# Kernel optimization log

Hardware: AMD Instinct MI355X
Metric: run time of the kernel (lower is better)

## Reference

```python
import jax, jax.numpy as jnp
import numpy as np

N, E, D, H = 50000, 800000, 128, 8
C = D // H  # per-head out_channels = 16
NEG_SLOPE = 0.2
EPS = 1e-5


def _layer_norm(x, w):
    mu = x.mean(-1, keepdims=True)
    var = ((x - mu) ** 2).mean(-1, keepdims=True)
    return (x - mu) / jnp.sqrt(var + EPS) * w


def setup_inputs() -> dict:
    key = jax.random.key(0)
    ks = jax.random.split(key, 9)
    s = 0.05  # weight init scale
    return {
        "x": jax.random.normal(ks[0], (N, D), dtype=jnp.float32),
        "edge_index": jax.random.randint(ks[1], (2, E), 0, N, dtype=jnp.int32),
        "edge_attr": jax.random.normal(ks[2], (E, D), dtype=jnp.float32),
        "ln1_w": jnp.ones((D,), jnp.float32),
        "lin_l_w": jax.random.normal(ks[3], (D, D), dtype=jnp.float32) * s,
        "lin_l_b": jnp.zeros((D,), jnp.float32),
        "lin_r_w": jax.random.normal(ks[4], (D, D), dtype=jnp.float32) * s,
        "lin_r_b": jnp.zeros((D,), jnp.float32),
        "lin_edge_w": jax.random.normal(ks[5], (D, D), dtype=jnp.float32) * s,
        "att": jax.random.normal(ks[6], (H, C), dtype=jnp.float32) * s,
        "attn_bias": jnp.zeros((D,), jnp.float32),
        "ln2_w": jnp.ones((D,), jnp.float32),
        "fc_w": jax.random.normal(ks[7], (4 * D, D), dtype=jnp.float32) * s,
        "proj_w": jax.random.normal(ks[8], (D, 4 * D), dtype=jnp.float32) * s,
    }


def reference(x, edge_index, edge_attr, ln1_w, lin_l_w, lin_l_b, lin_r_w,
              lin_r_b, lin_edge_w, att, attn_bias, ln2_w, fc_w, proj_w):
    n, d = x.shape
    h_heads, c = att.shape
    # --- GATv2Conv on ln_1(x) ---
    h = _layer_norm(x, ln1_w)
    xl = (h @ lin_l_w.T + lin_l_b).reshape(n, h_heads, c)  # source transform
    xr = (h @ lin_r_w.T + lin_r_b).reshape(n, h_heads, c)  # target transform
    e = (edge_attr @ lin_edge_w.T).reshape(-1, h_heads, c)  # [E,H,C]
    src, dst = edge_index[0], edge_index[1]
    z = jax.nn.leaky_relu(xl[src] + xr[dst] + e, NEG_SLOPE)  # [E,H,C]
    logits = jnp.einsum('ehc,hc->eh', z, att)  # [E,H]
    # segment softmax over destination nodes
    m = jax.lax.stop_gradient(jax.ops.segment_max(logits, dst, num_segments=n))
    num = jnp.exp(logits - m[dst])
    den = jax.ops.segment_sum(num, dst, num_segments=n)
    alpha = num / den[dst]  # [E,H]
    msg = xl[src] * alpha[..., None]  # [E,H,C]
    attn_out = jax.ops.segment_sum(msg, dst, num_segments=n).reshape(n, d) + attn_bias
    x = x + attn_out
    # --- MLP on ln_2(x) ---
    h2 = _layer_norm(x, ln2_w)
    x = x + jax.nn.relu(h2 @ fc_w.T) @ proj_w.T
    return x
```

## Files before the change

### kernel.cpp

```cpp
#include <hip/hip_runtime.h>

#define D 128
#define HEADS 8
#define CH 16
#define NEG 0.2f
#define LNEPS 1e-5f

typedef __attribute__((ext_vector_type(8))) short bf16x8;
typedef __attribute__((ext_vector_type(4))) float f32x4;

#define MFMA(a, b, c) __builtin_amdgcn_mfma_f32_16x16x32_bf16(a, b, c, 0, 0, 0)

__device__ __forceinline__ short f2bf(float f) {
    unsigned u = __builtin_bit_cast(unsigned, f);
    unsigned r = (u + 0x7fffu + ((u >> 16) & 1u)) >> 16;
    return (short)r;
}
__device__ __forceinline__ float bflo(unsigned u) {
    return __builtin_bit_cast(float, u << 16);
}
__device__ __forceinline__ float bfhi(unsigned u) {
    return __builtin_bit_cast(float, u & 0xffff0000u);
}
__device__ __forceinline__ bf16x8 pack8(f32x4 lo, f32x4 hi) {
    bf16x8 r;
    r[0] = f2bf(lo[0]); r[1] = f2bf(lo[1]); r[2] = f2bf(lo[2]); r[3] = f2bf(lo[3]);
    r[4] = f2bf(hi[0]); r[5] = f2bf(hi[1]); r[6] = f2bf(hi[2]); r[7] = f2bf(hi[3]);
    return r;
}

__global__ void convert_weights(const float* __restrict__ wl, const float* __restrict__ wr,
                                const float* __restrict__ we, const float* __restrict__ fc,
                                const float* __restrict__ pj, short* __restrict__ out) {
    int idx = blockIdx.x * 256 + threadIdx.x;
    float v;
    if (idx < 16384) v = wl[idx];
    else if (idx < 32768) v = wr[idx - 16384];
    else if (idx < 49152) v = we[idx - 32768];
    else if (idx < 114688) v = fc[idx - 49152];
    else if (idx < 180224) v = pj[idx - 114688];
    else return;
    out[idx] = f2bf(v);
}

__global__ void ln_kernel(const float* __restrict__ x, const float* __restrict__ w,
                          short* __restrict__ h, int n) {
    int row = blockIdx.x * 4 + (threadIdx.x >> 6);
    if (row >= n) return;
    int l = threadIdx.x & 63;
    long base = (long)row * D;
    float a = x[base + l], b = x[base + l + 64];
    float s = a + b, ss = a * a + b * b;
    #pragma unroll
    for (int m = 1; m < 64; m <<= 1) { s += __shfl_xor(s, m); ss += __shfl_xor(ss, m); }
    float mu = s * (1.0f / 128.0f);
    float var = ss * (1.0f / 128.0f) - mu * mu;
    float rstd = rsqrtf(var + LNEPS);
    h[base + l]      = f2bf((a - mu) * rstd * w[l]);
    h[base + l + 64] = f2bf((b - mu) * rstd * w[l + 64]);
}

__global__ __launch_bounds__(256) void node_lin_kernel(
        const short* __restrict__ h, const short* __restrict__ wl, const short* __restrict__ wr,
        const float* __restrict__ bl, const float* __restrict__ br,
        short* __restrict__ xl, short* __restrict__ xr, int n) {
    int wave = threadIdx.x >> 6, l = threadIdx.x & 63;
    int rbase = blockIdx.x * 64 + wave * 16;
    int g = l >> 4, c = l & 15;
    f32x4 acc[16];
    #pragma unroll
    for (int t = 0; t < 16; t++) acc[t] = (f32x4){0.f, 0.f, 0.f, 0.f};
    int arow = rbase + c;
    #pragma unroll
    for (int kk = 0; kk < 4; kk++) {
        int k0 = kk * 32 + g * 8;
        bf16x8 af = {};
        if (arow < n) af = *(const bf16x8*)(h + (long)arow * D + k0);
        #pragma unroll
        for (int t = 0; t < 16; t++) {
            const short* w = (t < 8) ? wl : wr;
            int col = (t & 7) * 16 + c;
            bf16x8 bf = *(const bf16x8*)(w + col * D + k0);
            acc[t] = MFMA(af, bf, acc[t]);
        }
    }
    #pragma unroll
    for (int t = 0; t < 16; t++) {
        int col = (t & 7) * 16 + c;
        short* out = (t < 8) ? xl : xr;
        float bias = (t < 8) ? bl[col] : br[col];
        #pragma unroll
        for (int r = 0; r < 4; r++) {
            int row = rbase + g * 4 + r;
            if (row < n) out[(long)row * D + col] = f2bf(acc[t][r] + bias);
        }
    }
}

__global__ void hist_kernel(const int* __restrict__ dst, int* __restrict__ counts, int nE) {
    int e = blockIdx.x * 256 + threadIdx.x;
    if (e < nE) atomicAdd(&counts[dst[e]], 1);
}

__global__ void scan1_kernel(const int* __restrict__ counts, int* __restrict__ offsets,
                             int* __restrict__ blocksum, int n) {
    __shared__ int sd[1024];
    int tid = threadIdx.x;
    int gid = blockIdx.x * 1024 + tid;
    int v = (gid < n) ? counts[gid] : 0;
    sd[tid] = v;
    __syncthreads();
    int acc = v;
    #pragma unroll
    for (int off = 1; off < 1024; off <<= 1) {
        int t = (tid >= off) ? sd[tid - off] : 0;
        __syncthreads();
        acc += t;
        sd[tid] = acc;
        __syncthreads();
    }
    if (gid < n) offsets[gid] = acc - v;
    if (tid == 1023) blocksum[blockIdx.x] = acc;
}

__global__ void scan2_kernel(int* __restrict__ blocksum, int nb) {
    __shared__ int sd[256];
    int tid = threadIdx.x;
    int v = (tid < nb) ? blocksum[tid] : 0;
    sd[tid] = v;
    __syncthreads();
    int acc = v;
    #pragma unroll
    for (int off = 1; off < 256; off <<= 1) {
        int t = (tid >= off) ? sd[tid - off] : 0;
        __syncthreads();
        acc += t;
        sd[tid] = acc;
        __syncthreads();
    }
    if (tid < nb) blocksum[tid] = acc - v;
}

__global__ void scan3_kernel(int* __restrict__ offsets, const int* __restrict__ blocksum,
                             int* __restrict__ cursor, int n) {
    int gid = blockIdx.x * 256 + threadIdx.x;
    if (gid < n) {
        int o = offsets[gid] + blocksum[gid >> 10];
        offsets[gid] = o;
        cursor[gid] = o;
    }
}

__global__ void place_kernel(const int* __restrict__ src, const int* __restrict__ dst,
                             int* __restrict__ cursor, int* __restrict__ src_perm,
                             int* __restrict__ dst_perm, int* __restrict__ eid_perm,
                             int nE) {
    int e = blockIdx.x * 256 + threadIdx.x;
    if (e < nE) {
        int d = dst[e];
        int pos = atomicAdd(&cursor[d], 1);
        src_perm[pos] = src[e];
        dst_perm[pos] = d;
        eid_perm[pos] = e;
    }
}

__global__ __launch_bounds__(256) void edge_kernel(
        const float* __restrict__ ea, const short* __restrict__ we,
        const int* __restrict__ src_perm, const int* __restrict__ dst_perm,
        const int* __restrict__ eid_perm,
        const short* __restrict__ xl, const short* __restrict__ xr,
        const float* __restrict__ att, float* __restrict__ num_perm,
        int nE, int ntiles, int nwaves) {
    __shared__ short wlds[16384];
    int tid = threadIdx.x;

    {
        int row = tid >> 1, half = tid & 1;
        const short* srow = we + row * D + half * 64;
        #pragma unroll
        for (int j = 0; j < 8; j++) {
            bf16x8 v = *(const bf16x8*)(srow + j * 8);
            int off = (half * 128 + j * 16) ^ ((row & 15) << 4);
            *(bf16x8*)((char*)wlds + row * 256 + off) = v;
        }
    }
    __syncthreads();

    int wave = tid >> 6, l = tid & 63;
    int el = l & 15, g = l >> 4;
    long ti = (long)blockIdx.x * 4 + wave;
    if (ti >= ntiles) return;

    int sp, dp;
    f32x4 ear[8];
    {
        long p0 = ti * 16 + el;
        long pc = (p0 < nE) ? p0 : (nE - 1);
        sp = src_perm[pc]; dp = dst_perm[pc];
        long ep = eid_perm[pc];
        const float* p = ea + ep * D + g * 8;
        ear[0] = *(const f32x4*)(p);       ear[1] = *(const f32x4*)(p + 4);
        ear[2] = *(const f32x4*)(p + 32);  ear[3] = *(const f32x4*)(p + 36);
        ear[4] = *(const f32x4*)(p + 64);  ear[5] = *(const f32x4*)(p + 68);
        ear[6] = *(const f32x4*)(p + 96);  ear[7] = *(const f32x4*)(p + 100);
    }

    for (; ti < ntiles; ti += nwaves) {
        long pcur = ti * 16 + el;
        bool valid = pcur < nE;
        int sc = sp, dc = dp;

        uint2 gl[8], gr[8];
        #pragma unroll
        for (int t = 0; t < 8; t++) {
            gl[t] = *(const uint2*)(xl + (long)sc * D + t * CH + g * 4);
            gr[t] = *(const uint2*)(xr + (long)dc * D + t * CH + g * 4);
        }

        long tin = ti + nwaves;
        long tcl = (tin < ntiles) ? tin : ti;
        long epn;
        {
            long pn = tcl * 16 + el;
            long pc = (pn < nE) ? pn : (nE - 1);
            sp = src_perm[pc]; dp = dst_perm[pc];
            epn = eid_perm[pc];
        }

        bf16x8 b0 = pack8(ear[0], ear[1]);
        bf16x8 b1 = pack8(ear[2], ear[3]);
        bf16x8 b2 = pack8(ear[4], ear[5]);
        bf16x8 b3 = pack8(ear[6], ear[7]);

        {
            const float* p = ea + epn * D + g * 8;
            ear[0] = *(const f32x4*)(p);       ear[1] = *(const f32x4*)(p + 4);
            ear[2] = *(const f32x4*)(p + 32);  ear[3] = *(const f32x4*)(p + 36);
            ear[4] = *(const f32x4*)(p + 64);  ear[5] = *(const f32x4*)(p + 68);
            ear[6] = *(const f32x4*)(p + 96);  ear[7] = *(const f32x4*)(p + 100);
        }

        f32x4 acc[8];
        #pragma unroll
        for (int t = 0; t < 8; t++) acc[t] = (f32x4){0.f, 0.f, 0.f, 0.f};
        #pragma unroll
        for (int kk = 0; kk < 4; kk++) {
            bf16x8 bb = (kk == 0) ? b0 : (kk == 1) ? b1 : (kk == 2) ? b2 : b3;
            #pragma unroll
            for (int t = 0; t < 8; t++) {
                int row = t * CH + el;
                int off = row * 256 + ((kk * 64 + g * 16) ^ ((row & 15) << 4));
                bf16x8 af = *(const bf16x8*)((char*)wlds + off);
                acc[t] = MFMA(af, bb, acc[t]);
            }
        }

        float logit[8];
        #pragma unroll
        for (int t = 0; t < 8; t++) {
            f32x4 av = *(const f32x4*)(att + t * CH + g * 4);
            float v0 = acc[t][0] + bflo(gl[t].x) + bflo(gr[t].x);
            float v1 = acc[t][1] + bfhi(gl[t].x) + bfhi(gr[t].x);
            float v2 = acc[t][2] + bflo(gl[t].y) + bflo(gr[t].y);
            float v3 = acc[t][3] + bfhi(gl[t].y) + bfhi(gr[t].y);
            v0 = v0 > 0.f ? v0 : NEG * v0;
            v1 = v1 > 0.f ? v1 : NEG * v1;
            v2 = v2 > 0.f ? v2 : NEG * v2;
            v3 = v3 > 0.f ? v3 : NEG * v3;
            float lg = v0 * av[0];
            lg = fmaf(v1, av[1], lg);
            lg = fmaf(v2, av[2], lg);
            lg = fmaf(v3, av[3], lg);
            lg += __shfl_xor(lg, 16);
            lg += __shfl_xor(lg, 32);
            logit[t] = lg;
        }
        if (g == 0 && valid) {
            float4 o0 = make_float4(__expf(logit[0]), __expf(logit[1]),
                                    __expf(logit[2]), __expf(logit[3]));
            float4 o1 = make_float4(__expf(logit[4]), __expf(logit[5]),
                                    __expf(logit[6]), __expf(logit[7]));
            *(float4*)(num_perm + pcur * HEADS) = o0;
            *(float4*)(num_perm + pcur * HEADS + 4) = o1;
        }
    }
}

__global__ __launch_bounds__(256) void aggregate_kernel(
        const int* __restrict__ src_perm, const int* __restrict__ offsets,
        const int* __restrict__ counts, const float* __restrict__ num_perm,
        const short* __restrict__ xl, const float* __restrict__ x,
        const float* __restrict__ ab, const float* __restrict__ w2,
        float* __restrict__ x_mid, short* __restrict__ h2, int n) {
    int node = blockIdx.x * 4 + (threadIdx.x >> 6);
    if (node >= n) return;
    int l = threadIdx.x & 63;
    int h = l >> 3;
    int start = offsets[node], cnt = counts[node];
    float a0 = 0.f, a1 = 0.f, den = 0.f;
    int i = 0;
    for (; i + 4 <= cnt; i += 4) {
        int s0 = src_perm[start + i],     s1 = src_perm[start + i + 1];
        int s2 = src_perm[start + i + 2], s3 = src_perm[start + i + 3];
        float n0 = num_perm[(long)(start + i) * HEADS + h];
        float n1 = num_perm[(long)(start + i + 1) * HEADS + h];
        float n2 = num_perm[(long)(start + i + 2) * HEADS + h];
        float n3 = num_perm[(long)(start + i + 3) * HEADS + h];
        unsigned u0 = *(const unsigned*)(xl + (long)s0 * D + 2 * l);
        unsigned u1 = *(const unsigned*)(xl + (long)s1 * D + 2 * l);
        unsigned u2 = *(const unsigned*)(xl + (long)s2 * D + 2 * l);
        unsigned u3 = *(const unsigned*)(xl + (long)s3 * D + 2 * l);
        a0 = fmaf(bflo(u0), n0, a0); a1 = fmaf(bfhi(u0), n0, a1);
        a0 = fmaf(bflo(u1), n1, a0); a1 = fmaf(bfhi(u1), n1, a1);
        a0 = fmaf(bflo(u2), n2, a0); a1 = fmaf(bfhi(u2), n2, a1);
        a0 = fmaf(bflo(u3), n3, a0); a1 = fmaf(bfhi(u3), n3, a1);
        den += n0 + n1 + n2 + n3;
    }
    for (; i < cnt; i++) {
        float nm = num_perm[(long)(start + i) * HEADS + h];
        int s = src_perm[start + i];
        unsigned u = *(const unsigned*)(xl + (long)s * D + 2 * l);
        a0 = fmaf(bflo(u), nm, a0);
        a1 = fmaf(bfhi(u), nm, a1);
        den += nm;
    }
    float rden = cnt > 0 ? 1.f / den : 0.f;
    a0 *= rden; a1 *= rden;
    long base = (long)node * D;
    float2 xv = *(const float2*)(x + base + 2 * l);
    float2 abv = *(const float2*)(ab + 2 * l);
    float xm0 = xv.x + a0 + abv.x;
    float xm1 = xv.y + a1 + abv.y;
    *(float2*)(x_mid + base + 2 * l) = make_float2(xm0, xm1);
    float s_ = xm0 + xm1, ss = xm0 * xm0 + xm1 * xm1;
    #pragma unroll
    for (int m = 1; m < 64; m <<= 1) { s_ += __shfl_xor(s_, m); ss += __shfl_xor(ss, m); }
    float mu = s_ * (1.0f / 128.0f);
    float var = ss * (1.0f / 128.0f) - mu * mu;
    float rstd = rsqrtf(var + LNEPS);
    float2 wv = *(const float2*)(w2 + 2 * l);
    h2[base + 2 * l]     = f2bf((xm0 - mu) * rstd * wv.x);
    h2[base + 2 * l + 1] = f2bf((xm1 - mu) * rstd * wv.y);
}

__global__ __launch_bounds__(256) void fcproj_kernel(
        const short* __restrict__ h2, const short* __restrict__ wfc,
        const short* __restrict__ wpj, const float* __restrict__ x_mid,
        float* __restrict__ out, int n) {
    __shared__ char tl[65536];
    int wave = threadIdx.x >> 6, l = threadIdx.x & 63;
    int rbase = blockIdx.x * 64 + wave * 16;
    int g = l >> 4, c = l & 15;
    int arow = rbase + c;

    #pragma unroll
    for (int half = 0; half < 2; half++) {
        f32x4 acc[16];
        #pragma unroll
        for (int t = 0; t < 16; t++) acc[t] = (f32x4){0.f, 0.f, 0.f, 0.f};
        #pragma unroll
        for (int kk = 0; kk < 4; kk++) {
            int k0 = kk * 32 + g * 8;
            bf16x8 af = {};
            if (arow < n) af = *(const bf16x8*)(h2 + (long)arow * D + k0);
            #pragma unroll
            for (int t = 0; t < 16; t++) {
                int col = half * 256 + t * 16 + c;
                bf16x8 bf = *(const bf16x8*)(wfc + (long)col * D + k0);
                acc[t] = MFMA(af, bf, acc[t]);
            }
        }
        #pragma unroll
        for (int t = 0; t < 16; t++) {
            int col = half * 256 + t * 16 + c;
            #pragma unroll
            for (int r = 0; r < 4; r++) {
                int lr = wave * 16 + g * 4 + r;
                float v = acc[t][r];
                int addr = lr * 1024 + ((2 * col) ^ ((lr & 7) << 4));
                *(short*)(tl + addr) = f2bf(v > 0.f ? v : 0.f);
            }
        }
    }
    __syncthreads();

    f32x4 pacc[8];
    #pragma unroll
    for (int t = 0; t < 8; t++) pacc[t] = (f32x4){0.f, 0.f, 0.f, 0.f};
    int lr = wave * 16 + c;
    #pragma unroll
    for (int kk = 0; kk < 16; kk++) {
        int k0 = kk * 32 + g * 8;
        int addr = lr * 1024 + ((2 * k0) ^ ((lr & 7) << 4));
        bf16x8 af = *(const bf16x8*)(tl + addr);
        #pragma unroll
        for (int t = 0; t < 8; t++) {
            bf16x8 bf = *(const bf16x8*)(wpj + (long)(t * 16 + c) * 512 + k0);
            pacc[t] = MFMA(af, bf, pacc[t]);
        }
    }
    #pragma unroll
    for (int t = 0; t < 8; t++) {
        int col = t * 16 + c;
        #pragma unroll
        for (int r = 0; r < 4; r++) {
            int row = rbase + g * 4 + r;
            if (row < n) out[(long)row * D + col] = x_mid[(long)row * D + col] + pacc[t][r];
        }
    }
}

extern "C" void kernel_launch(void* const* d_in, const int* in_sizes, int n_in,
                              void* d_out, int out_size, void* d_ws, size_t ws_size,
                              hipStream_t stream) {
    const float* x    = (const float*)d_in[0];
    const int*   eidx = (const int*)d_in[1];
    const float* ea   = (const float*)d_in[2];
    const float* ln1w = (const float*)d_in[3];
    const float* wl   = (const float*)d_in[4];
    const float* bl   = (const float*)d_in[5];
    const float* wr   = (const float*)d_in[6];
    const float* br   = (const float*)d_in[7];
    const float* we   = (const float*)d_in[8];
    const float* att  = (const float*)d_in[9];
    const float* ab   = (const float*)d_in[10];
    const float* ln2w = (const float*)d_in[11];
    const float* wfc  = (const float*)d_in[12];
    const float* wpj  = (const float*)d_in[13];
    int N = in_sizes[0] / D;
    int E = in_sizes[1] / 2;
    const int* srcp = eidx;
    const int* dstp = eidx + E;

    char* ws = (char*)d_ws;
    size_t NB2 = (size_t)N * D * 2;
    size_t NB4 = (size_t)N * D * 4;
    size_t E84 = (size_t)E * HEADS * 4;
    size_t o = 0;
    short* xl_bf   = (short*)(ws + o); o += NB2;
    short* xr_bf   = (short*)(ws + o); o += NB2;
    float* numperm = (float*)(ws + o); o += E84;
    float* xmid    = (float*)(ws + o); o += NB4;
    short* hbuf    = (short*)(ws + o); o += NB2;
    short* wbf     = (short*)(ws + o); o += 180224 * 2;
    int* counts    = (int*)(ws + o);   o += (size_t)N * 4;
    int* offsets   = (int*)(ws + o);   o += (size_t)N * 4;
    int* cursor    = (int*)(ws + o);   o += (size_t)N * 4;
    int* src_perm  = (int*)(ws + o);   o += (size_t)E * 4;
    int* dst_perm  = (int*)(ws + o);   o += (size_t)E * 4;
    int* eid_perm  = (int*)(ws + o);   o += (size_t)E * 4;
    int* blocksum  = (int*)(ws + o);   o += 256 * 4;

    int nb = (N + 1023) / 1024;
    int ntiles = (E + 15) / 16;
    int egrid = 1280;
    int nwaves = egrid * 4;

    hipMemsetAsync(counts, 0, (size_t)N * 4, stream);

    convert_weights<<<704, 256, 0, stream>>>(wl, wr, we, wfc, wpj, wbf);
    ln_kernel<<<(N + 3) / 4, 256, 0, stream>>>(x, ln1w, hbuf, N);
    node_lin_kernel<<<(N + 63) / 64, 256, 0, stream>>>(hbuf, wbf, wbf + 16384,
                                                       bl, br, xl_bf, xr_bf, N);
    hist_kernel<<<(E + 255) / 256, 256, 0, stream>>>(dstp, counts, E);
    scan1_kernel<<<nb, 1024, 0, stream>>>(counts, offsets, blocksum, N);
    scan2_kernel<<<1, 256, 0, stream>>>(blocksum, nb);
    scan3_kernel<<<(N + 255) / 256, 256, 0, stream>>>(offsets, blocksum, cursor, N);
    place_kernel<<<(E + 255) / 256, 256, 0, stream>>>(srcp, dstp, cursor, src_perm,
                                                      dst_perm, eid_perm, E);
    edge_kernel<<<egrid, 256, 0, stream>>>(ea, wbf + 32768, src_perm, dst_perm,
                                           eid_perm, xl_bf, xr_bf, att,
                                           numperm, E, ntiles, nwaves);
    aggregate_kernel<<<(N + 3) / 4, 256, 0, stream>>>(src_perm, offsets, counts,
                                                      numperm, xl_bf, x, ab, ln2w,
                                                      xmid, hbuf, N);
    fcproj_kernel<<<(N + 63) / 64, 256, 0, stream>>>(hbuf, wbf + 49152,
                                                     wbf + 114688, xmid,
                                                     (float*)d_out, N);
}
```

Baseline: 518.7 us.

## Relayout LDS tiles into MFMA fragment order and shrink fcproj blocks

The edge kernel now stores the edge-weight matrix in LDS in MFMA fragment order, so each fragment read is a contiguous 16-byte access with simple address arithmetic. The attention vector is hoisted into registers once per wave instead of being reloaded every tile. The fcproj kernel moves to 128-thread blocks with a private 16 KB LDS region per wave stored in fragment order, which removes the block-wide barrier and halves LDS per block to allow more resident blocks. The cost is more fcproj blocks, each reloading the weights from global memory, and the loss of the old XOR swizzle, which may cause bank conflicts on the scattered 2-byte LDS writes.

```diff
diff --git a/kernel.cpp b/kernel.cpp
--- a/kernel.cpp
+++ b/kernel.cpp
@@ -175,15 +175,12 @@
     __shared__ short wlds[16384];
     int tid = threadIdx.x;
 
-    {
-        int row = tid >> 1, half = tid & 1;
-        const short* srow = we + row * D + half * 64;
-        #pragma unroll
-        for (int j = 0; j < 8; j++) {
-            bf16x8 v = *(const bf16x8*)(srow + j * 8);
-            int off = (half * 128 + j * 16) ^ ((row & 15) << 4);
-            *(bf16x8*)((char*)wlds + row * 256 + off) = v;
-        }
+    #pragma unroll
+    for (int q = 0; q < 8; q++) {
+        int d16 = tid * 8 + q;
+        int gq = d16 & 3, elq = (d16 >> 2) & 15, kkq = (d16 >> 6) & 3, tq = d16 >> 8;
+        bf16x8 v = *(const bf16x8*)(we + (tq * 16 + elq) * D + kkq * 32 + gq * 8);
+        *(bf16x8*)((char*)wlds + d16 * 16) = v;
     }
     __syncthreads();
 
@@ -191,6 +188,10 @@
     int el = l & 15, g = l >> 4;
     long ti = (long)blockIdx.x * 4 + wave;
     if (ti >= ntiles) return;
+
+    f32x4 av[8];
+    #pragma unroll
+    for (int t = 0; t < 8; t++) av[t] = *(const f32x4*)(att + t * CH + g * 4);
 
     int sp, dp;
     f32x4 ear[8];
@@ -249,8 +250,7 @@
             bf16x8 bb = (kk == 0) ? b0 : (kk == 1) ? b1 : (kk == 2) ? b2 : b3;
             #pragma unroll
             for (int t = 0; t < 8; t++) {
-                int row = t * CH + el;
-                int off = row * 256 + ((kk * 64 + g * 16) ^ ((row & 15) << 4));
+                int off = ((t * 4 + kk) << 10) + (el << 6) + (g << 4);
                 bf16x8 af = *(const bf16x8*)((char*)wlds + off);
                 acc[t] = MFMA(af, bb, acc[t]);
             }
@@ -259,7 +259,6 @@
         float logit[8];
         #pragma unroll
         for (int t = 0; t < 8; t++) {
-            f32x4 av = *(const f32x4*)(att + t * CH + g * 4);
             float v0 = acc[t][0] + bflo(gl[t].x) + bflo(gr[t].x);
             float v1 = acc[t][1] + bfhi(gl[t].x) + bfhi(gr[t].x);
             float v2 = acc[t][2] + bflo(gl[t].y) + bflo(gr[t].y);
@@ -268,10 +267,10 @@
             v1 = v1 > 0.f ? v1 : NEG * v1;
             v2 = v2 > 0.f ? v2 : NEG * v2;
             v3 = v3 > 0.f ? v3 : NEG * v3;
-            float lg = v0 * av[0];
-            lg = fmaf(v1, av[1], lg);
-            lg = fmaf(v2, av[2], lg);
-            lg = fmaf(v3, av[3], lg);
+            float lg = v0 * av[t][0];
+            lg = fmaf(v1, av[t][1], lg);
+            lg = fmaf(v2, av[t][2], lg);
+            lg = fmaf(v3, av[t][3], lg);
             lg += __shfl_xor(lg, 16);
             lg += __shfl_xor(lg, 32);
             logit[t] = lg;
@@ -344,15 +343,16 @@
     h2[base + 2 * l + 1] = f2bf((xm1 - mu) * rstd * wv.y);
 }
 
-__global__ __launch_bounds__(256) void fcproj_kernel(
+__global__ __launch_bounds__(128) void fcproj_kernel(
         const short* __restrict__ h2, const short* __restrict__ wfc,
         const short* __restrict__ wpj, const float* __restrict__ x_mid,
         float* __restrict__ out, int n) {
-    __shared__ char tl[65536];
+    __shared__ char tl[32768];
     int wave = threadIdx.x >> 6, l = threadIdx.x & 63;
-    int rbase = blockIdx.x * 64 + wave * 16;
+    int rbase = blockIdx.x * 32 + wave * 16;
     int g = l >> 4, c = l & 15;
     int arow = rbase + c;
+    char* tw = tl + wave * 16384;
 
     #pragma unroll
     for (int half = 0; half < 2; half++) {
@@ -374,26 +374,25 @@
         #pragma unroll
         for (int t = 0; t < 16; t++) {
             int col = half * 256 + t * 16 + c;
+            int kk_p = col >> 5, g_p = (col >> 3) & 3, e_p = col & 7;
             #pragma unroll
             for (int r = 0; r < 4; r++) {
-                int lr = wave * 16 + g * 4 + r;
+                int rr = g * 4 + r;
                 float v = acc[t][r];
-                int addr = lr * 1024 + ((2 * col) ^ ((lr & 7) << 4));
-                *(short*)(tl + addr) = f2bf(v > 0.f ? v : 0.f);
+                int addr = ((kk_p * 16 + rr) * 4 + g_p) * 16 + e_p * 2;
+                *(short*)(tw + addr) = f2bf(v > 0.f ? v : 0.f);
             }
         }
     }
-    __syncthreads();
 
     f32x4 pacc[8];
     #pragma unroll
     for (int t = 0; t < 8; t++) pacc[t] = (f32x4){0.f, 0.f, 0.f, 0.f};
-    int lr = wave * 16 + c;
     #pragma unroll
     for (int kk = 0; kk < 16; kk++) {
         int k0 = kk * 32 + g * 8;
-        int addr = lr * 1024 + ((2 * k0) ^ ((lr & 7) << 4));
-        bf16x8 af = *(const bf16x8*)(tl + addr);
+        int addr = ((kk * 16 + c) * 4 + g) * 16;
+        bf16x8 af = *(const bf16x8*)(tw + addr);
         #pragma unroll
         for (int t = 0; t < 8; t++) {
             bf16x8 bf = *(const bf16x8*)(wpj + (long)(t * 16 + c) * 512 + k0);
@@ -475,7 +474,7 @@
     aggregate_kernel<<<(N + 3) / 4, 256, 0, stream>>>(src_perm, offsets, counts,
                                                       numperm, xl_bf, x, ab, ln2w,
                                                       xmid, hbuf, N);
-    fcproj_kernel<<<(N + 63) / 64, 256, 0, stream>>>(hbuf, wbf + 49152,
+    fcproj_kernel<<<(N + 31) / 32, 128, 0, stream>>>(hbuf, wbf + 49152,
                                                      wbf + 114688, xmid,
                                                      (float*)d_out, N);
 }
```

Measured after the change: 534.1 us. 3.0% more time.
